# Performance work log

Measured on AMD Instinct MI355X. Metric: run time of the kernel, lower is better.

## Reference

```python
import jax, jax.numpy as jnp
import numpy as np

# ---- configuration (matches init_kwargs) ----
IH, IW, IC, OC = 32, 32, 8, 16
KH = KW = 3
STRIDE = (1, 1)
PAD = (1, 1)
DIL = (1, 1)
P = 5                       # num_gp_pts per GP neuron
I_DIM = IC * KH * KW        # 72 = kernel_input_size
OH = (IH + 2 * PAD[0] - DIL[0] * (KH - 1) - 1) // STRIDE[0] + 1
OW = (IW + 2 * PAD[1] - DIL[1] * (KW - 1) - 1) // STRIDE[1] + 1
JITTER = 1e-4


def setup_inputs() -> dict:
    key = jax.random.key(0)
    k1, k2, k3, k4, k5 = jax.random.split(key, 5)
    N = 8
    x_mean = jax.random.normal(k1, (N, IH, IW, IC), jnp.float32)
    # variances must be positive
    x_var = 0.1 + 0.9 * jax.random.uniform(k2, (N, IH, IW, IC), jnp.float32)
    # inducing inputs: spread on [-1,1] with small perturbation (well-conditioned K)
    base = jnp.linspace(-1.0, 1.0, P, dtype=jnp.float32)
    z = base[None, None, :] + 0.05 * jax.random.normal(k3, (OC, I_DIM, P), jnp.float32)
    h = jax.random.normal(k4, (OC, I_DIM, P), jnp.float32)      # inducing outputs
    raw_l = jax.random.uniform(k5, (OC, I_DIM), jnp.float32)    # pre-softplus lengthscale
    return {"x_mean": x_mean, "x_var": x_var, "z": z, "h": h, "raw_l": raw_l}


def im2col(img):
    """[N,IH,IW,C] NHWC -> [N*L, C*KH*KW], torch.nn.Unfold ordering (channel slowest)."""
    x = jnp.transpose(img, (0, 3, 1, 2))  # NCHW, matches the torch transposes
    patches = jax.lax.conv_general_dilated_patches(
        x, (KH, KW), STRIDE, [(PAD[0], PAD[0]), (PAD[1], PAD[1])], rhs_dilation=DIL
    )  # [N, C*KH*KW, OH, OW], feature dim channel-major like torch unfold
    Nb = patches.shape[0]
    return patches.reshape(Nb, I_DIM, OH * OW).transpose(0, 2, 1).reshape(Nb * OH * OW, I_DIM)


def gp_layer(mu, s2, z, h, raw_l):
    """GP-neuron (KAN-style) moment propagation.
    mu, s2: [R, I]; z, h: [O, I, P]; raw_l: [O, I].
    Per neuron (o,i): SE kernel k(a,b)=exp(-(a-b)^2/(2 l^2)), unit signal variance.
    Under x_i ~ N(mu_i, s2_i):
      q_p   = sqrt(l^2/(l^2+s2)) * exp(-(mu-z_p)^2 / (2 (l^2+s2)))   (expected kernel)
      mean  = q . K^{-1} h
      var   = 1 - q . K^{-1} q
    Layer output (KAN sum over inputs): y_o = sum_i f_oi(x_i).
    """
    l2 = jax.nn.softplus(raw_l) ** 2                                  # [O,I]
    dz = z[:, :, :, None] - z[:, :, None, :]                          # [O,I,P,P]
    K = jnp.exp(-0.5 * dz**2 / l2[:, :, None, None]) + JITTER * jnp.eye(P, dtype=mu.dtype)
    Kinv = jnp.linalg.inv(K)                                          # [O,I,P,P] (tiny)
    alpha = jnp.einsum('oipq,oiq->oip', Kinv, h)                      # [O,I,P]

    d = l2[None, :, :, None] + s2[:, None, :, None]                   # [R,O,I,1]
    diff = mu[:, None, :, None] - z[None]                             # [R,O,I,P]
    q = jnp.sqrt(l2[None, :, :, None] / d) * jnp.exp(-0.5 * diff**2 / d)  # [R,O,I,P]

    out_mean = jnp.einsum('roip,oip->ro', q, alpha)                   # [R,O]
    qK = jnp.einsum('roip,oipq->roiq', q, Kinv)                       # [R,O,I,P]
    qKq = jnp.einsum('roiq,roiq->ro', qK, q)                          # [R,O]
    # sum_i (k(x,x) - q K^{-1} q) with k(x,x)=1 -> I - sum_i qKq_i
    out_var = jnp.maximum(jnp.asarray(mu.shape[1], mu.dtype) - qKq, 1e-6)
    return out_mean, out_var


def reference(x_mean, x_var, z, h, raw_l):
    N = x_mean.shape[0]
    mu = im2col(x_mean)                  # [N*L, I]
    s2 = im2col(x_var)                   # [N*L, I]
    m, v = gp_layer(mu, s2, z, h, raw_l)
    # col2im: [N*L, OC] -> [N, OH, OW, OC]
    return m.reshape(N, OH, OW, OC), v.reshape(N, OH, OW, OC)
```

## Files before the change

kernel.cpp:

```cpp
#include <hip/hip_runtime.h>
#include <math.h>

#define OC_N   16
#define I_DIM  72
#define PN     5
#define NEU    (OC_N * I_DIM)
#define NF     32
#define RTOT   8192
#define OUT_HALF (RTOT * OC_N)
#define LOG2E  1.4426950408889634f
#define RLOG2E 0.6931471805599453f

#if __has_builtin(__builtin_amdgcn_rcpf)
#define RCPF(x) __builtin_amdgcn_rcpf(x)
#else
#define RCPF(x) (1.0f / (x))
#endif
#if __has_builtin(__builtin_amdgcn_exp2f)
#define EXP2F(x) __builtin_amdgcn_exp2f(x)
#else
#define EXP2F(x) exp2f(x)
#endif
#if __has_builtin(__builtin_amdgcn_logf)
#define LOG2F(x) __builtin_amdgcn_logf(x)
#else
#define LOG2F(x) log2f(x)
#endif


__global__ __launch_bounds__(256) void gp_prep_kernel(
    const float* __restrict__ zin, const float* __restrict__ hin,
    const float* __restrict__ rlin, float* __restrict__ nr) {
  int idx = blockIdx.x * blockDim.x + threadIdx.x;
  if (idx >= NEU) return;
  float x  = rlin[idx];
  float t  = EXP2F(-fabsf(x) * LOG2E);
  float sp = fmaxf(x, 0.0f) + LOG2F(1.0f + t) * RLOG2E;
  float l2 = sp * sp;
  float cexp = -0.5f * LOG2E * RCPF(l2);

  float zz[PN], hh[PN];
#pragma unroll
  for (int p = 0; p < PN; ++p) {
    zz[p] = zin[idx * PN + p];
    hh[p] = hin[idx * PN + p];
  }
  float A[PN][PN], B[PN][PN];
#pragma unroll
  for (int p = 0; p < PN; ++p) {
#pragma unroll
    for (int q = 0; q < PN; ++q) {
      float dz = zz[p] - zz[q];
      A[p][q] = EXP2F(cexp * dz * dz);
      B[p][q] = (p == q) ? 1.0f : 0.0f;
    }
  }
#pragma unroll
  for (int p = 0; p < PN; ++p) A[p][p] += 1e-4f;

#pragma unroll
  for (int c = 0; c < PN; ++c) {
    float pivinv = RCPF(A[c][c]);
#pragma unroll
    for (int j = 0; j < PN; ++j) { A[c][j] *= pivinv; B[c][j] *= pivinv; }
#pragma unroll
    for (int r = 0; r < PN; ++r) {
      if (r == c) continue;
      float f = A[r][c];
#pragma unroll
      for (int j = 0; j < PN; ++j) { A[r][j] -= f * A[c][j]; B[r][j] -= f * B[c][j]; }
    }
  }
  float alpha[PN];
#pragma unroll
  for (int p = 0; p < PN; ++p) {
    float s = 0.0f;
#pragma unroll
    for (int q = 0; q < PN; ++q) s += B[p][q] * hh[q];
    alpha[p] = s;
  }
  float* o = nr + idx * NF;
  o[0] = l2;
  o[1] = 0.0f;
#pragma unroll
  for (int p = 0; p < PN; ++p) {
    o[2 + p]  = zz[p];
    o[7 + p]  = alpha[p];
    o[12 + p] = B[p][p];
  }
  int j = 17;
#pragma unroll
  for (int p = 0; p < PN; ++p)
#pragma unroll
    for (int q = p + 1; q < PN; ++q) o[j++] = 2.0f * B[p][q];
  o[27] = o[28] = o[29] = o[30] = o[31] = 0.0f;
}

__global__ __launch_bounds__(576) void gp_fused_kernel(
    const float* __restrict__ xm, const float* __restrict__ xv,
    const float* __restrict__ nr, float* __restrict__ out) {
  const int tx = threadIdx.x;
  const int k  = __builtin_amdgcn_readfirstlane(threadIdx.y);
  const int o  = blockIdx.y;
  const int r  = blockIdx.x * 64 + tx;
  const int n  = r >> 10;
  const int pix = r & 1023;
  const int oh = pix >> 5;
  const int ow = pix & 31;
  const float* nb = nr + o * (I_DIM * NF);

  const int kh = k / 3;
  const int kw = k - kh * 3;
  const int ih = oh + kh - 1;
  const int iw = ow + kw - 1;
  const bool vld = ((unsigned)ih < 32u) & ((unsigned)iw < 32u);

  float mu[8], s2[8];
  if (vld) {
    const int base = ((n * 32 + ih) * 32 + iw) * 8;
    const float4 a0 = *(const float4*)(xm + base);
    const float4 a1 = *(const float4*)(xm + base + 4);
    const float4 b0 = *(const float4*)(xv + base);
    const float4 b1 = *(const float4*)(xv + base + 4);
    mu[0]=a0.x; mu[1]=a0.y; mu[2]=a0.z; mu[3]=a0.w;
    mu[4]=a1.x; mu[5]=a1.y; mu[6]=a1.z; mu[7]=a1.w;
    s2[0]=b0.x; s2[1]=b0.y; s2[2]=b0.z; s2[3]=b0.w;
    s2[4]=b1.x; s2[5]=b1.y; s2[6]=b1.z; s2[7]=b1.w;
  } else {
#pragma unroll
    for (int c = 0; c < 8; ++c) { mu[c] = 0.0f; s2[c] = 0.0f; }
  }

  float mean_acc = 0.0f;
  float qkq_acc  = 0.0f;
#pragma unroll
  for (int c = 0; c < 8; ++c) {
    const float* p = nb + (c * 9 + k) * NF;
    const float l2    = p[0];
    const float d     = l2 + s2[c];
    const float inv_d = RCPF(d);
    const float coef2 = l2 * inv_d;
    const float coef  = sqrtf(coef2);
    const float el    = -0.72134752044f * inv_d;
    const float m     = mu[c];
    const float d0 = m - p[2];
    const float d1 = m - p[3];
    const float d2 = m - p[4];
    const float d3 = m - p[5];
    const float d4 = m - p[6];
    const float u0 = EXP2F(el * d0 * d0);
    const float u1 = EXP2F(el * d1 * d1);
    const float u2 = EXP2F(el * d2 * d2);
    const float u3 = EXP2F(el * d3 * d3);
    const float u4 = EXP2F(el * d4 * d4);
    const float dotA =
        fmaf(u0, p[7], fmaf(u1, p[8], fmaf(u2, p[9], fmaf(u3, p[10], u4 * p[11]))));
    const float t0 = fmaf(p[12], u0, fmaf(p[17], u1, fmaf(p[18], u2, fmaf(p[19], u3, p[20] * u4))));
    const float t1 = fmaf(p[13], u1, fmaf(p[21], u2, fmaf(p[22], u3, p[23] * u4)));
    const float t2 = fmaf(p[14], u2, fmaf(p[24], u3, p[25] * u4));
    const float t3 = fmaf(p[15], u3, p[26] * u4);
    const float t4 = p[16] * u4;
    const float quad =
        fmaf(u0, t0, fmaf(u1, t1, fmaf(u2, t2, fmaf(u3, t3, u4 * t4))));
    mean_acc = fmaf(coef, dotA, mean_acc);
    qkq_acc  = fmaf(coef2, quad, qkq_acc);
  }

  __shared__ float2 red[9][64];
  red[threadIdx.y][tx] = make_float2(mean_acc, qkq_acc);
  __syncthreads();
  if (threadIdx.y == 0) {
    float m = mean_acc;
    float q = qkq_acc;
#pragma unroll
    for (int s = 1; s < 9; ++s) {
      const float2 v = red[s][tx];
      m += v.x;
      q += v.y;
    }
    const int i = r * OC_N + o;
    out[i] = m;
    out[OUT_HALF + i] = fmaxf(72.0f - q, 1e-6f);
  }
}

extern "C" void kernel_launch(void* const* d_in, const int* in_sizes, int n_in,
                              void* d_out, int out_size, void* d_ws, size_t ws_size,
                              hipStream_t stream) {
  const float* xm = (const float*)d_in[0];
  const float* xv = (const float*)d_in[1];
  const float* z  = (const float*)d_in[2];
  const float* h  = (const float*)d_in[3];
  const float* rl = (const float*)d_in[4];
  float* out = (float*)d_out;
  float* nr  = (float*)d_ws;

  gp_prep_kernel<<<dim3((NEU + 255) / 256), dim3(256), 0, stream>>>(z, h, rl, nr);

  dim3 grid(RTOT / 64, OC_N);
  dim3 block(64, 9);
  gp_fused_kernel<<<grid, block, 0, stream>>>(xm, xv, nr, out);
}
```

Measured before the change: 86.66 us.

## Remap lanes to channel-per-thread with register-resident neuron params and shuffle reduction

Each thread now owns one input channel c for a fixed kernel offset k and keeps that neuron's 27 parameters in registers. It loops over 8 groups of 8 rows and reduces across the 8 channels with xor shuffles before writing partial sums to shared memory. Before, each thread looped over channels and did scalar/global loads of parameters per channel. This is meant to cut repeated parameter loads and make the loads uniform per lane. In exchange, input loads become scalar 4-byte gathers instead of float4, and there are extra shuffle operations.

```diff
diff --git a/kernel.cpp b/kernel.cpp
--- a/kernel.cpp
+++ b/kernel.cpp
@@ -99,88 +99,86 @@
 __global__ __launch_bounds__(576) void gp_fused_kernel(
     const float* __restrict__ xm, const float* __restrict__ xv,
     const float* __restrict__ nr, float* __restrict__ out) {
-  const int tx = threadIdx.x;
-  const int k  = __builtin_amdgcn_readfirstlane(threadIdx.y);
-  const int o  = blockIdx.y;
-  const int r  = blockIdx.x * 64 + tx;
-  const int n  = r >> 10;
-  const int pix = r & 1023;
-  const int oh = pix >> 5;
-  const int ow = pix & 31;
-  const float* nb = nr + o * (I_DIM * NF);
-
-  const int kh = k / 3;
-  const int kw = k - kh * 3;
-  const int ih = oh + kh - 1;
-  const int iw = ow + kw - 1;
-  const bool vld = ((unsigned)ih < 32u) & ((unsigned)iw < 32u);
-
-  float mu[8], s2[8];
-  if (vld) {
-    const int base = ((n * 32 + ih) * 32 + iw) * 8;
-    const float4 a0 = *(const float4*)(xm + base);
-    const float4 a1 = *(const float4*)(xm + base + 4);
-    const float4 b0 = *(const float4*)(xv + base);
-    const float4 b1 = *(const float4*)(xv + base + 4);
-    mu[0]=a0.x; mu[1]=a0.y; mu[2]=a0.z; mu[3]=a0.w;
-    mu[4]=a1.x; mu[5]=a1.y; mu[6]=a1.z; mu[7]=a1.w;
-    s2[0]=b0.x; s2[1]=b0.y; s2[2]=b0.z; s2[3]=b0.w;
-    s2[4]=b1.x; s2[5]=b1.y; s2[6]=b1.z; s2[7]=b1.w;
-  } else {
-#pragma unroll
-    for (int c = 0; c < 8; ++c) { mu[c] = 0.0f; s2[c] = 0.0f; }
-  }
-
-  float mean_acc = 0.0f;
-  float qkq_acc  = 0.0f;
-#pragma unroll
-  for (int c = 0; c < 8; ++c) {
-    const float* p = nb + (c * 9 + k) * NF;
-    const float l2    = p[0];
-    const float d     = l2 + s2[c];
+  const int tx  = threadIdx.x;
+  const int rlo = tx >> 3;
+  const int c   = tx & 7;
+  const int k   = __builtin_amdgcn_readfirstlane(threadIdx.y);
+  const int kh  = k / 3;
+  const int kw  = k - kh * 3;
+  const int o   = blockIdx.y;
+  const int rbase = blockIdx.x * 64;
+
+  const float* rec = nr + (o * I_DIM + (c * 9 + k)) * NF;
+  float P[27];
+#pragma unroll
+  for (int j = 0; j < 27; ++j) P[j] = rec[j];
+
+  const float l2    = P[0];
+  __shared__ float2 red[9][64];
+
+#pragma unroll
+  for (int it = 0; it < 8; ++it) {
+    const int r8  = rbase + it * 8;
+    const int n   = r8 >> 10;
+    const int pix = r8 & 1023;
+    const int oh  = pix >> 5;
+    const int ow0 = pix & 31;
+    const int ih  = oh + kh - 1;
+    const int iw  = ow0 + rlo + kw - 1;
+    const bool valid = ((unsigned)ih < 32u) & ((unsigned)iw < 32u);
+    const int ihc = ih < 0 ? 0 : (ih > 31 ? 31 : ih);
+    const int iwc = iw < 0 ? 0 : (iw > 31 ? 31 : iw);
+    const int addr = ((n * 32 + ihc) * 32 + iwc) * 8 + c;
+    float m  = xm[addr];
+    float s2 = xv[addr];
+    m  = valid ? m  : 0.0f;
+    s2 = valid ? s2 : 0.0f;
+
+    const float d     = l2 + s2;
     const float inv_d = RCPF(d);
     const float coef2 = l2 * inv_d;
     const float coef  = sqrtf(coef2);
     const float el    = -0.72134752044f * inv_d;
-    const float m     = mu[c];
-    const float d0 = m - p[2];
-    const float d1 = m - p[3];
-    const float d2 = m - p[4];
-    const float d3 = m - p[5];
-    const float d4 = m - p[6];
+    const float d0 = m - P[2];
+    const float d1 = m - P[3];
+    const float d2 = m - P[4];
+    const float d3 = m - P[5];
+    const float d4 = m - P[6];
     const float u0 = EXP2F(el * d0 * d0);
     const float u1 = EXP2F(el * d1 * d1);
     const float u2 = EXP2F(el * d2 * d2);
     const float u3 = EXP2F(el * d3 * d3);
     const float u4 = EXP2F(el * d4 * d4);
     const float dotA =
-        fmaf(u0, p[7], fmaf(u1, p[8], fmaf(u2, p[9], fmaf(u3, p[10], u4 * p[11]))));
-    const float t0 = fmaf(p[12], u0, fmaf(p[17], u1, fmaf(p[18], u2, fmaf(p[19], u3, p[20] * u4))));
-    const float t1 = fmaf(p[13], u1, fmaf(p[21], u2, fmaf(p[22], u3, p[23] * u4)));
-    const float t2 = fmaf(p[14], u2, fmaf(p[24], u3, p[25] * u4));
-    const float t3 = fmaf(p[15], u3, p[26] * u4);
-    const float t4 = p[16] * u4;
+        fmaf(u0, P[7], fmaf(u1, P[8], fmaf(u2, P[9], fmaf(u3, P[10], u4 * P[11]))));
+    const float t0 = fmaf(P[12], u0, fmaf(P[17], u1, fmaf(P[18], u2, fmaf(P[19], u3, P[20] * u4))));
+    const float t1 = fmaf(P[13], u1, fmaf(P[21], u2, fmaf(P[22], u3, P[23] * u4)));
+    const float t2 = fmaf(P[14], u2, fmaf(P[24], u3, P[25] * u4));
+    const float t3 = fmaf(P[15], u3, P[26] * u4);
+    const float t4 = P[16] * u4;
     const float quad =
         fmaf(u0, t0, fmaf(u1, t1, fmaf(u2, t2, fmaf(u3, t3, u4 * t4))));
-    mean_acc = fmaf(coef, dotA, mean_acc);
-    qkq_acc  = fmaf(coef2, quad, qkq_acc);
-  }
-
-  __shared__ float2 red[9][64];
-  red[threadIdx.y][tx] = make_float2(mean_acc, qkq_acc);
+    float mean = coef * dotA;
+    float qkq  = coef2 * quad;
+
+    mean += __shfl_xor(mean, 1); qkq += __shfl_xor(qkq, 1);
+    mean += __shfl_xor(mean, 2); qkq += __shfl_xor(qkq, 2);
+    mean += __shfl_xor(mean, 4); qkq += __shfl_xor(qkq, 4);
+    if (c == 0) red[k][it * 8 + rlo] = make_float2(mean, qkq);
+  }
+
   __syncthreads();
   if (threadIdx.y == 0) {
-    float m = mean_acc;
-    float q = qkq_acc;
-#pragma unroll
-    for (int s = 1; s < 9; ++s) {
+    float msum = 0.0f, qsum = 0.0f;
+#pragma unroll
+    for (int s = 0; s < 9; ++s) {
       const float2 v = red[s][tx];
-      m += v.x;
-      q += v.y;
+      msum += v.x;
+      qsum += v.y;
     }
-    const int i = r * OC_N + o;
-    out[i] = m;
-    out[OUT_HALF + i] = fmaxf(72.0f - q, 1e-6f);
+    const int i = (rbase + tx) * OC_N + o;
+    out[i] = msum;
+    out[OUT_HALF + i] = fmaxf(72.0f - qsum, 1e-6f);
   }
 }
 
```

After: 99.54 us. +14.9%, slower.
